# Optimization experiments

Measured on AMD Instinct MI355X. Metric: run time of the kernel, lower is better.

## Reference

```python
import jax, jax.numpy as jnp
import numpy as np
from jax import lax

B, S, Q, A, L = 8192, 8192, 64, 1024, 3
H = 64  # post-processor hidden


def setup_inputs() -> dict:
    key = jax.random.key(0)
    ks = jax.random.split(key, 9)
    state = jax.random.normal(ks[0], (B, S), dtype=jnp.float32)
    enc_w = jax.random.normal(ks[1], (Q, S), dtype=jnp.float32) * (1.0 / np.sqrt(S))
    enc_b = jnp.zeros((Q,), dtype=jnp.float32)
    quantum_params = jax.random.normal(ks[2], (L, Q, 3), dtype=jnp.float32) * 0.1
    measurement_ops = jax.random.normal(ks[3], (A, Q, 2), dtype=jnp.float32) * 0.1
    w1 = jax.random.normal(ks[4], (H, A), dtype=jnp.float32) * (1.0 / np.sqrt(A))
    b1 = jnp.zeros((H,), dtype=jnp.float32)
    w2 = jax.random.normal(ks[5], (A, H), dtype=jnp.float32) * (1.0 / np.sqrt(H))
    b2 = jnp.zeros((A,), dtype=jnp.float32)
    return {"state": state, "enc_w": enc_w, "enc_b": enc_b,
            "quantum_params": quantum_params, "measurement_ops": measurement_ops,
            "w1": w1, "b1": b1, "w2": w2, "b2": b2}


def reference(state, enc_w, enc_b, quantum_params, measurement_ops, w1, b1, w2, b2):
    # Encode: Linear + softmax. quantum_state = complex(encoded, 0); since every
    # rotation is a real scaling (qs*cos + roll(qs)*sin), the imaginary part
    # stays identically zero, so we track only the real component.
    encoded = jax.nn.softmax(state @ enc_w.T + enc_b, axis=-1)  # [B, Q]

    # Rotation gates applied sequentially in layer -> qubit -> (x,y,z) order,
    # which is exactly the row-major flattening of quantum_params.
    thetas = quantum_params.reshape(-1)  # [L*Q*3]

    def gate(qs, theta):
        c = jnp.cos(theta * 0.5)
        s = jnp.sin(theta * 0.5)
        return qs * c + jnp.roll(qs, 1, axis=-1) * s, None

    qs, _ = lax.scan(gate, encoded, thetas)  # [B, Q]

    # Measurement: torch.sum has no dim -> reduces over batch AND qubit dims.
    # imag == 0, so the ops[:, :, 1] term contributes nothing.
    measurements = jnp.einsum('bq,aq->a', qs, measurement_ops[:, :, 0])  # [A]

    # Post-processor MLP on the [A] vector.
    h = jax.nn.relu(measurements @ w1.T + b1)
    return h @ w2.T + b2  # [A]
```

## Files before the change

### kernel.cpp

```cpp
#include <hip/hip_runtime.h>
#include <hip/hip_fp16.h>

typedef __fp16 h2_t __attribute__((ext_vector_type(2)));
typedef _Float16 f16x8 __attribute__((ext_vector_type(8)));
typedef float f32x4 __attribute__((ext_vector_type(4)));
typedef unsigned int uint32;

#define S_DIM 8192
#define B_DIM 8192
#define Q_DIM 64
#define A_DIM 1024
#define H_DIM 64
#define N_GATES 576

#define MT 64
#define KSPLIT 8
#define KC (S_DIM / KSPLIT)
#define BK 64
#define NSTEP (KC / BK)
#define NCHUNK 4
#define CHUNK (N_GATES / NCHUNK)

__device__ __forceinline__ uint32 pk_f16(float x, float y) {
    h2_t h = __builtin_amdgcn_cvt_pkrtz(x, y);
    return __builtin_bit_cast(uint32, h);
}

__device__ __forceinline__ f32x4 mfma16(uint4 a, uint4 b, f32x4 c) {
    return __builtin_amdgcn_mfma_f32_16x16x32_f16(
        __builtin_bit_cast(f16x8, a), __builtin_bit_cast(f16x8, b), c, 0, 0, 0);
}

__device__ __forceinline__ void gload_lds16(const float* g, float* lds) {
    __builtin_amdgcn_global_load_lds(
        (const __attribute__((address_space(1))) void*)g,
        (__attribute__((address_space(3))) void*)lds, 16, 0, 0);
}

__global__ void k_pre(const float* __restrict__ encw, uint4* __restrict__ bpack,
                      const float* __restrict__ w1, const float* __restrict__ mo,
                      float* __restrict__ WM) {
    const int bid = blockIdx.x;
    const int t   = threadIdx.x;
    if (bid < 256) {
        const int gid  = bid * 256 + t;
        const int lane = gid & 63;
        const int nt   = (gid >> 6) & 3;
        const int kt   = gid >> 8;
        const int n = nt * 16 + (lane & 15);
        const int k = kt * 32 + (lane >> 4) * 8;
        const float* p = encw + (size_t)n * S_DIM + k;
        float4 x0 = *(const float4*)p;
        float4 x1 = *(const float4*)(p + 4);
        uint4 r;
        r.x = pk_f16(x0.x, x0.y);
        r.y = pk_f16(x0.z, x0.w);
        r.z = pk_f16(x1.x, x1.y);
        r.w = pk_f16(x1.z, x1.w);
        bpack[gid] = r;
    } else {
        __shared__ float red[4][64];
        const int j    = bid - 256;
        const int lane = t & 63;
        const int wv   = t >> 6;
        const float* w1r = w1 + (size_t)j * A_DIM + wv * 256;
        const float* mop = mo + (size_t)wv * 256 * 128 + lane * 2;
        float acc = 0.f;
        for (int a = 0; a < 256; ++a)
            acc = fmaf(w1r[a], mop[(size_t)a * 128], acc);
        red[wv][lane] = acc;
        __syncthreads();
        if (t < 64)
            WM[(size_t)j * 64 + t] = red[0][t] + red[1][t] + red[2][t] + red[3][t];
    }
}

__global__ __launch_bounds__(256, 4) void k_gemm(
        const float* __restrict__ state, const uint4* __restrict__ bpack,
        float* __restrict__ partial) {
    __shared__ __align__(16) float As[2][MT * BK];
    const int t  = threadIdx.x;
    const int w  = t >> 6;
    const int l  = t & 63;
    const int m0 = blockIdx.x * MT;
    const int ks = blockIdx.y;
    const int k0 = ks * KC;

    const uint4* pb = bpack + (size_t)(k0 >> 5) * 4 * 64 + l;

    const int fr = w * 16 + (l & 15);
    const int g2 = l >> 4;
    const int fx = fr & 15;

#define DMA(BUF, S) do { \
        _Pragma("unroll") \
        for (int i = 0; i < 4; ++i) { \
            const int rl = (w * 4 + i) * 4 + (l >> 4); \
            const int ss = (l & 15) ^ (rl & 15); \
            const float* gp = state + (size_t)(m0 + rl) * S_DIM + k0 + (S) * BK + ss * 4; \
            gload_lds16(gp, &As[BUF][(w * 4 + i) * 256]); \
        } } while (0)

    f32x4 acc[4] = {};

    DMA(0, 0);

    for (int s = 0; s < NSTEP; ++s) {
        const int cur = s & 1;
        uint4 bf0[4], bf1[4];
#pragma unroll
        for (int nt = 0; nt < 4; ++nt) {
            bf0[nt] = pb[(size_t)((s * 2 + 0) * 4 + nt) * 64];
            bf1[nt] = pb[(size_t)((s * 2 + 1) * 4 + nt) * 64];
        }
        asm volatile("s_waitcnt vmcnt(8)" ::: "memory");
        __builtin_amdgcn_s_barrier();
        __builtin_amdgcn_sched_barrier(0);
        if (s + 1 < NSTEP) DMA(cur ^ 1, s + 1);
        const int b0 = fr * BK;
        const float4 f00 = *(const float4*)&As[cur][b0 + (((2 * g2 + 0) ^ fx) << 2)];
        const float4 f01 = *(const float4*)&As[cur][b0 + (((2 * g2 + 1) ^ fx) << 2)];
        const float4 f10 = *(const float4*)&As[cur][b0 + (((8 + 2 * g2 + 0) ^ fx) << 2)];
        const float4 f11 = *(const float4*)&As[cur][b0 + (((8 + 2 * g2 + 1) ^ fx) << 2)];
        uint4 af0, af1;
        af0.x = pk_f16(f00.x, f00.y); af0.y = pk_f16(f00.z, f00.w);
        af0.z = pk_f16(f01.x, f01.y); af0.w = pk_f16(f01.z, f01.w);
        af1.x = pk_f16(f10.x, f10.y); af1.y = pk_f16(f10.z, f10.w);
        af1.z = pk_f16(f11.x, f11.y); af1.w = pk_f16(f11.z, f11.w);
#pragma unroll
        for (int nt = 0; nt < 4; ++nt) {
            acc[nt] = mfma16(af0, bf0[nt], acc[nt]);
            acc[nt] = mfma16(af1, bf1[nt], acc[nt]);
        }
    }
#undef DMA

    float* pc = partial + (size_t)ks * (B_DIM * Q_DIM);
    const int mr = m0 + w * 16 + (l >> 4) * 4;
    const int nc = l & 15;
#pragma unroll
    for (int nt = 0; nt < 4; ++nt)
#pragma unroll
        for (int r = 0; r < 4; ++r)
            pc[(size_t)(mr + r) * Q_DIM + nt * 16 + nc] = acc[nt][r];
}

__global__ void k_softmax(const float* __restrict__ partial,
                          const float* __restrict__ encb,
                          float* __restrict__ colsum_parts) {
    __shared__ float red[4][64];
    const int lane = threadIdx.x & 63;
    const int wv   = threadIdx.x >> 6;
    const float eb = encb[lane];
    float accq = 0.f;
    for (int i = 0; i < 8; ++i) {
        const int r = blockIdx.x * 32 + i * 4 + wv;
        float x = eb;
#pragma unroll
        for (int ks = 0; ks < KSPLIT; ++ks)
            x += partial[(size_t)ks * (B_DIM * Q_DIM) + (size_t)r * Q_DIM + lane];
        float m = x;
        for (int o = 32; o > 0; o >>= 1) m = fmaxf(m, __shfl_xor(m, o));
        float e = __expf(x - m);
        float s = e;
        for (int o = 32; o > 0; o >>= 1) s += __shfl_xor(s, o);
        accq += e / s;
    }
    red[wv][lane] = accq;
    __syncthreads();
    if (threadIdx.x < 64) {
        colsum_parts[blockIdx.x * 64 + lane] =
            red[0][lane] + red[1][lane] + red[2][lane] + red[3][lane];
    }
}

__global__ void k_final(const float* __restrict__ colsum_parts,
                        const float* __restrict__ qp,
                        const float* __restrict__ WM,
                        const float* __restrict__ b1,
                        const float* __restrict__ w2, const float* __restrict__ b2,
                        float* __restrict__ out) {
    __shared__ float red[4][64];
    __shared__ float t0[64];
    __shared__ float cs[N_GATES], ss[N_GATES];
    __shared__ float pA[NCHUNK][64];
    __shared__ float pB[2][64];
    __shared__ float fv[64];
    __shared__ float gv[64];
    __shared__ float hl[64];
    const int t    = threadIdx.x;
    const int lane = t & 63;
    const int wv   = t >> 6;

    for (int g = t; g < N_GATES; g += 256) {
        float th = qp[g] * 0.5f;
        cs[g] = __cosf(th);
        ss[g] = __sinf(th);
    }
    {
        float c = 0.f;
#pragma unroll
        for (int i = 0; i < 64; ++i)
            c += colsum_parts[(size_t)(wv * 64 + i) * 64 + lane];
        red[wv][lane] = c;
    }
    __syncthreads();
    if (t < 64)
        t0[t] = red[0][t] + red[1][t] + red[2][t] + red[3][t];
    {
        float p = (lane == 0) ? 1.f : 0.f;
        const int g0 = wv * CHUNK;
        for (int g = 0; g < CHUNK; ++g) {
            float prev = __shfl(p, (lane + 63) & 63);
            p = fmaf(cs[g0 + g], p, ss[g0 + g] * prev);
        }
        pA[wv][lane] = p;
    }
    __syncthreads();
    if (wv < 2) {
        float r = 0.f;
        for (int i = 0; i < 64; ++i)
            r += pA[2 * wv][i] * pA[2 * wv + 1][(lane - i) & 63];
        pB[wv][lane] = r;
    }
    __syncthreads();
    if (wv == 0) {
        float r = 0.f;
        for (int i = 0; i < 64; ++i)
            r += pB[0][i] * pB[1][(lane - i) & 63];
        fv[lane] = r;
    }
    __syncthreads();
    if (wv == 0) {
        float r = 0.f;
        for (int i = 0; i < 64; ++i)
            r += fv[i] * t0[(lane - i) & 63];
        gv[lane] = r;
    }
    __syncthreads();
    if (t < 64) {
        float v = 0.f;
        const float* wr = WM + (size_t)t * 64;
#pragma unroll
        for (int q = 0; q < 64; ++q)
            v = fmaf(wr[q], gv[q], v);
        hl[t] = fmaxf(v + b1[t], 0.f);
    }
    __syncthreads();
    const int a = blockIdx.x * 4 + wv;
    float v = w2[(size_t)a * H_DIM + lane] * hl[lane];
    for (int o = 32; o > 0; o >>= 1) v += __shfl_xor(v, o);
    if (lane == 0) out[a] = v + b2[a];
}

extern "C" void kernel_launch(void* const* d_in, const int* in_sizes, int n_in,
                              void* d_out, int out_size, void* d_ws, size_t ws_size,
                              hipStream_t stream) {
    const float* state = (const float*)d_in[0];
    const float* encw  = (const float*)d_in[1];
    const float* encb  = (const float*)d_in[2];
    const float* qp    = (const float*)d_in[3];
    const float* mo    = (const float*)d_in[4];
    const float* w1    = (const float*)d_in[5];
    const float* b1    = (const float*)d_in[6];
    const float* w2    = (const float*)d_in[7];
    const float* b2    = (const float*)d_in[8];
    float* out = (float*)d_out;

    float* ws           = (float*)d_ws;
    float* colsum_parts = ws;
    float* partial      = ws + 16384;
    float* WM           = partial + (size_t)KSPLIT * B_DIM * Q_DIM;
    uint4* bpack        = (uint4*)(WM + 4096);

    k_pre<<<dim3(320), dim3(256), 0, stream>>>(encw, bpack, w1, mo, WM);
    k_gemm<<<dim3(B_DIM / MT, KSPLIT), dim3(256), 0, stream>>>(state, bpack, partial);
    k_softmax<<<dim3(256), dim3(256), 0, stream>>>(partial, encb, colsum_parts);
    k_final<<<dim3(256), dim3(256), 0, stream>>>(colsum_parts, qp, WM, b1, w2, b2, out);
}
```

Before: 95.72 us.

## Triple-buffer GEMM with B operand staged through LDS and smaller K tile

```diff
diff --git a/kernel.cpp b/kernel.cpp
--- a/kernel.cpp
+++ b/kernel.cpp
@@ -16,7 +16,7 @@
 #define MT 64
 #define KSPLIT 8
 #define KC (S_DIM / KSPLIT)
-#define BK 64
+#define BK 32
 #define NSTEP (KC / BK)
 #define NCHUNK 4
 #define CHUNK (N_GATES / NCHUNK)
@@ -66,6 +66,7 @@
         const float* w1r = w1 + (size_t)j * A_DIM + wv * 256;
         const float* mop = mo + (size_t)wv * 256 * 128 + lane * 2;
         float acc = 0.f;
+#pragma unroll 8
         for (int a = 0; a < 256; ++a)
             acc = fmaf(w1r[a], mop[(size_t)a * 128], acc);
         red[wv][lane] = acc;
@@ -78,7 +79,8 @@
 __global__ __launch_bounds__(256, 4) void k_gemm(
         const float* __restrict__ state, const uint4* __restrict__ bpack,
         float* __restrict__ partial) {
-    __shared__ __align__(16) float As[2][MT * BK];
+    __shared__ __align__(16) float As[3][MT * BK];
+    __shared__ __align__(16) float Bs[3][4 * 256];
     const int t  = threadIdx.x;
     const int w  = t >> 6;
     const int l  = t & 63;
@@ -86,54 +88,61 @@
     const int ks = blockIdx.y;
     const int k0 = ks * KC;
 
-    const uint4* pb = bpack + (size_t)(k0 >> 5) * 4 * 64 + l;
-
     const int fr = w * 16 + (l & 15);
+    const int fx = fr & 7;
     const int g2 = l >> 4;
-    const int fx = fr & 15;
 
 #define DMA(BUF, S) do { \
         _Pragma("unroll") \
-        for (int i = 0; i < 4; ++i) { \
-            const int rl = (w * 4 + i) * 4 + (l >> 4); \
-            const int ss = (l & 15) ^ (rl & 15); \
+        for (int i = 0; i < 2; ++i) { \
+            const int j_ = 2 * w + i; \
+            const int rl = j_ * 8 + (l >> 3); \
+            const int ss = (l & 7) ^ (l >> 3); \
             const float* gp = state + (size_t)(m0 + rl) * S_DIM + k0 + (S) * BK + ss * 4; \
-            gload_lds16(gp, &As[BUF][(w * 4 + i) * 256]); \
+            gload_lds16(gp, &As[BUF][j_ * 256]); \
+        } \
+        { \
+            const float* gb = (const float*)(bpack + (size_t)((k0 >> 5) + (S)) * 256 + w * 64 + l); \
+            gload_lds16(gb, &Bs[BUF][w * 256]); \
         } } while (0)
 
+#define COMPUTE(BUF, S) do { \
+        const int b0 = fr * BK; \
+        const float4 f0 = *(const float4*)&As[BUF][b0 + (((2 * g2 + 0) ^ fx) << 2)]; \
+        const float4 f1 = *(const float4*)&As[BUF][b0 + (((2 * g2 + 1) ^ fx) << 2)]; \
+        uint4 af; \
+        af.x = pk_f16(f0.x, f0.y); af.y = pk_f16(f0.z, f0.w); \
+        af.z = pk_f16(f1.x, f1.y); af.w = pk_f16(f1.z, f1.w); \
+        const uint4 bf0 = *(const uint4*)&Bs[BUF][0 * 256 + l * 4]; \
+        const uint4 bf1 = *(const uint4*)&Bs[BUF][1 * 256 + l * 4]; \
+        const uint4 bf2 = *(const uint4*)&Bs[BUF][2 * 256 + l * 4]; \
+        const uint4 bf3 = *(const uint4*)&Bs[BUF][3 * 256 + l * 4]; \
+        acc[0] = mfma16(af, bf0, acc[0]); \
+        acc[1] = mfma16(af, bf1, acc[1]); \
+        acc[2] = mfma16(af, bf2, acc[2]); \
+        acc[3] = mfma16(af, bf3, acc[3]); } while (0)
+
     f32x4 acc[4] = {};
 
     DMA(0, 0);
-
-    for (int s = 0; s < NSTEP; ++s) {
-        const int cur = s & 1;
-        uint4 bf0[4], bf1[4];
-#pragma unroll
-        for (int nt = 0; nt < 4; ++nt) {
-            bf0[nt] = pb[(size_t)((s * 2 + 0) * 4 + nt) * 64];
-            bf1[nt] = pb[(size_t)((s * 2 + 1) * 4 + nt) * 64];
-        }
-        asm volatile("s_waitcnt vmcnt(8)" ::: "memory");
+    DMA(1, 1);
+
+    int buf = 0, ibuf = 2;
+    for (int s = 0; s < NSTEP - 1; ++s) {
+        asm volatile("s_waitcnt vmcnt(3)" ::: "memory");
         __builtin_amdgcn_s_barrier();
         __builtin_amdgcn_sched_barrier(0);
-        if (s + 1 < NSTEP) DMA(cur ^ 1, s + 1);
-        const int b0 = fr * BK;
-        const float4 f00 = *(const float4*)&As[cur][b0 + (((2 * g2 + 0) ^ fx) << 2)];
-        const float4 f01 = *(const float4*)&As[cur][b0 + (((2 * g2 + 1) ^ fx) << 2)];
-        const float4 f10 = *(const float4*)&As[cur][b0 + (((8 + 2 * g2 + 0) ^ fx) << 2)];
-        const float4 f11 = *(const float4*)&As[cur][b0 + (((8 + 2 * g2 + 1) ^ fx) << 2)];
-        uint4 af0, af1;
-        af0.x = pk_f16(f00.x, f00.y); af0.y = pk_f16(f00.z, f00.w);
-        af0.z = pk_f16(f01.x, f01.y); af0.w = pk_f16(f01.z, f01.w);
-        af1.x = pk_f16(f10.x, f10.y); af1.y = pk_f16(f10.z, f10.w);
-        af1.z = pk_f16(f11.x, f11.y); af1.w = pk_f16(f11.z, f11.w);
-#pragma unroll
-        for (int nt = 0; nt < 4; ++nt) {
-            acc[nt] = mfma16(af0, bf0[nt], acc[nt]);
-            acc[nt] = mfma16(af1, bf1[nt], acc[nt]);
-        }
-    }
+        if (s + 2 < NSTEP) DMA(ibuf, s + 2);
+        COMPUTE(buf, s);
+        buf  = (buf  == 2) ? 0 : buf  + 1;
+        ibuf = (ibuf == 2) ? 0 : ibuf + 1;
+    }
+    asm volatile("s_waitcnt vmcnt(0)" ::: "memory");
+    __builtin_amdgcn_s_barrier();
+    __builtin_amdgcn_sched_barrier(0);
+    COMPUTE(buf, NSTEP - 1);
 #undef DMA
+#undef COMPUTE
 
     float* pc = partial + (size_t)ks * (B_DIM * Q_DIM);
     const int mr = m0 + w * 16 + (l >> 4) * 4;
```

Result: faster. 86.90 us (median of 2 runs) (-9.2%).
